# Performance work log

Measured on AMD Instinct MI355X. Metric: run time of the kernel, lower is better.

## Reference

```python
import jax, jax.numpy as jnp
import numpy as np
from jax import lax

DN = ('NCHW', 'OIHW', 'NCHW')


def setup_inputs() -> dict:
    key = jax.random.key(0)
    k1, k2, k3, k4, k5, k6 = jax.random.split(key, 6)
    B, Ch, H, W = 16, 256, 32, 32   # two feature maps of 256 ch -> c = 512
    C = 2 * Ch
    return {
        'x1': jax.random.normal(k1, (B, Ch, H, W), dtype=jnp.float32),
        'x2': jax.random.normal(k2, (B, Ch, H, W), dtype=jnp.float32),
        'g_w': jax.random.normal(k3, (C, C, 3, 3), dtype=jnp.float32) * 0.02,
        'w_w': jax.random.normal(k4, (256, C, 1, 1), dtype=jnp.float32) * 0.05,
        'weight1': jax.random.normal(k5, (C, 16), dtype=jnp.float32) * 0.1,
        'weight2': jax.random.normal(k6, (C, 16), dtype=jnp.float32) * 0.1,
    }


def reference(x1, x2, g_w, w_w, weight1, weight2):
    x = jnp.concatenate([x1, x2], axis=1)            # [b, c, h, w]
    b, c, h, w = x.shape
    g_x = lax.conv_general_dilated(x, g_w, (1, 1), 'SAME', dimension_numbers=DN)
    value = g_x.reshape(b, c, h * w)                 # [b, c, n]
    q = x.reshape(b, c, h * w)                       # query == key source
    sim = jnp.einsum('bcn,bdn->bcd', q, q) * (float(c) ** -0.5)  # [b, c, c]
    random_map = weight1 @ weight2.T                 # [c, c]
    attn = jax.nn.softmax(sim + random_map[None], axis=-1)
    ctx = jnp.einsum('bcd,bdn->bcn', attn, value).reshape(b, c, h, w)
    out = lax.conv_general_dilated(ctx, w_w, (1, 1), 'VALID', dimension_numbers=DN)
    return out
```

## Files before the change

### kernel.cpp

```cpp
#include <hip/hip_runtime.h>
#include <math.h>

typedef float f32x4 __attribute__((ext_vector_type(4)));
typedef short s16x8 __attribute__((ext_vector_type(8)));
typedef unsigned int u32;
typedef unsigned short u16;
typedef u16 u16x4 __attribute__((ext_vector_type(4)));

static constexpr size_t OFF_XT    = 0;
static constexpr size_t OFF_XQ    = 4734976;
static constexpr size_t OFF_ATTNT = 4734976;
static constexpr size_t OFF_WATTN = 6832128;
static constexpr size_t OFF_P0    = 8929280;
static constexpr size_t OFF_P1    = 11026432;
static constexpr size_t OFF_VT    = 8929280;
static constexpr size_t OFF_WA    = 13123584;
static constexpr size_t OFF_RM    = 14303232;
static constexpr size_t OFF_WWB   = 14565376;

__device__ __forceinline__ u16 f2bf(float f) {
    u32 u = __float_as_uint(f);
    u32 r = (u + 0x7FFFu + ((u >> 16) & 1u)) >> 16;
    return (u16)r;
}
__device__ __forceinline__ float bf2f(u16 v) {
    return __uint_as_float(((u32)v) << 16);
}

__device__ __forceinline__ void gload_lds16(const void* g, void* l) {
    __builtin_amdgcn_global_load_lds(
        (const u32 __attribute__((address_space(1)))*)(uintptr_t)g,
        (u32 __attribute__((address_space(3)))*)(uintptr_t)l, 16, 0, 0);
}

__global__ __launch_bounds__(256) void prep_kernel(const float* __restrict__ x1,
                                                   const float* __restrict__ x2,
                                                   const float* __restrict__ gw,
                                                   const float* __restrict__ ww,
                                                   const float* __restrict__ w1,
                                                   const float* __restrict__ w2,
                                                   float* __restrict__ rm,
                                                   u16* __restrict__ wA,
                                                   u16* __restrict__ wwb,
                                                   u16* __restrict__ xT,
                                                   u16* __restrict__ xq) {
    __shared__ __attribute__((aligned(16))) u32 shm[4608];
    const int t = threadIdx.x;
    const int bid = blockIdx.x;

    if (bid < 512) {
        const int co = bid;
        const float* g = gw + (size_t)co * 4608;
        float* lf = (float*)shm;
#pragma unroll
        for (int i = 0; i < 18; ++i) lf[t + i * 256] = g[t + i * 256];
        __syncthreads();
        u16* dst = wA + (size_t)co * 4608;
#pragma unroll
        for (int i = 0; i < 18; ++i) {
            int k = t + i * 256;
            int r = k >> 9, ci = k & 511;
            dst[k] = f2bf(lf[ci * 9 + r]);
        }
    } else if (bid < 2560) {
        int xid = bid - 512;
        int nt = xid & 15;
        int cit = (xid >> 4) & 7;
        int b = xid >> 7;
        int n0 = nt * 64, ci0 = cit * 64;
        const float* src = (ci0 < 256) ? (x1 + ((size_t)(b * 256 + ci0)) * 1024)
                                       : (x2 + ((size_t)(b * 256 + ci0 - 256)) * 1024);
        u16* xqb = xq + ((size_t)(b * 512 + ci0)) * 1024;
        u16* lt = (u16*)shm;
#pragma unroll
        for (int p4 = 0; p4 < 4; ++p4) {
            int ch = (t >> 4) + p4 * 16;
            int px = (t & 15) * 4;
            float4 v = *(const float4*)&src[(size_t)ch * 1024 + n0 + px];
            u16x4 pk = {f2bf(v.x), f2bf(v.y), f2bf(v.z), f2bf(v.w)};
            *(u16x4*)&xqb[(size_t)ch * 1024 + n0 + px] = pk;
            lt[(px + 0) * 65 + ch] = pk[0];
            lt[(px + 1) * 65 + ch] = pk[1];
            lt[(px + 2) * 65 + ch] = pk[2];
            lt[(px + 3) * 65 + ch] = pk[3];
        }
        __syncthreads();
        {
            int px_l = t >> 2, c16 = (t & 3) * 16;
            int n = n0 + px_l;
            int y = n >> 5, x = n & 31;
            int p = (y + 1) * 34 + (x + 1);
            u16* dst = xT + ((size_t)b * 1156 + p) * 512 + ci0 + c16;
            *(s16x8*)&dst[0] = *(const s16x8*)&lt[px_l * 65 + c16];
            *(s16x8*)&dst[8] = *(const s16x8*)&lt[px_l * 65 + c16 + 8];
        }
    } else if (bid < 2576) {
        int b = bid - 2560;
        u16* base = xT + (size_t)b * 1156 * 512;
        s16x8 z = {0, 0, 0, 0, 0, 0, 0, 0};
        for (int idx = t; idx < 132 * 64; idx += 256) {
            int row = idx >> 6, seg = idx & 63;
            int p;
            if (row < 34) p = row;
            else if (row < 68) p = 1122 + (row - 34);
            else if (row < 100) p = (row - 67) * 34;
            else p = (row - 99) * 34 + 33;
            *(s16x8*)&base[(size_t)p * 512 + seg * 8] = z;
        }
    } else if (bid < 3600) {
        int idx = (bid - 2576) * 256 + t;
        int c = idx >> 9, d = idx & 511;
        float s = 0.f;
#pragma unroll
        for (int k = 0; k < 16; ++k) s = fmaf(w1[c * 16 + k], w2[d * 16 + k], s);
        rm[idx] = s;
    } else {
        int idx = (bid - 3600) * 256 + t;
        float4 v = ((const float4*)ww)[idx];
        u16x4 pk = {f2bf(v.x), f2bf(v.y), f2bf(v.z), f2bf(v.w)};
        *(u16x4*)&wwb[(size_t)idx * 4] = pk;
    }
}

__global__ __launch_bounds__(256) void sim_part(const u16* __restrict__ xq,
                                                u16* __restrict__ simP) {
    __shared__ __attribute__((aligned(16))) u16 smem[128 * 128];
    u16* As = smem;
    u16* Bs = smem + 128 * 64;
    const int b = blockIdx.z, m0 = blockIdx.y * 128;
    const int n0 = (blockIdx.x & 3) * 128, khalf = blockIdx.x >> 2;
    const int t = threadIdx.x, w = t >> 6, l = t & 63;
    const u16* xb = xq + (size_t)b * 512 * 1024 + khalf * 512;

    const u16 *agp[4], *bgp[4];
    u16 *ald[4], *bld[4];
#pragma unroll
    for (int i = 0; i < 4; ++i) {
        int rr = w * 8 + i * 32 + (l >> 3);
        int gi = (l & 7) ^ (rr & 7);
        agp[i] = xb + (size_t)(m0 + rr) * 1024 + gi * 8;
        bgp[i] = xb + (size_t)(n0 + rr) * 1024 + gi * 8;
        ald[i] = &As[(w * 8 + i * 32) * 64];
        bld[i] = &Bs[(w * 8 + i * 32) * 64];
    }

    f32x4 acc[4][4] = {};
    const int wm = (w >> 1) * 64, wn = (w & 1) * 64;

    for (int kt = 0; kt < 8; ++kt) {
        int ko = kt << 6;
        if (kt) __syncthreads();
#pragma unroll
        for (int i = 0; i < 4; ++i) gload_lds16(agp[i] + ko, ald[i]);
#pragma unroll
        for (int i = 0; i < 4; ++i) gload_lds16(bgp[i] + ko, bld[i]);
        __syncthreads();
#pragma unroll
        for (int kk = 0; kk < 2; ++kk) {
            int gbase = kk * 4 + (l >> 4);
            s16x8 af[4], bf[4];
#pragma unroll
            for (int i = 0; i < 4; ++i) {
                int row = wm + i * 16 + (l & 15);
                af[i] = *(const s16x8*)&As[row * 64 + ((gbase ^ (row & 7)) << 3)];
            }
#pragma unroll
            for (int j = 0; j < 4; ++j) {
                int row = wn + j * 16 + (l & 15);
                bf[j] = *(const s16x8*)&Bs[row * 64 + ((gbase ^ (row & 7)) << 3)];
            }
#pragma unroll
            for (int i = 0; i < 4; ++i)
#pragma unroll
                for (int j = 0; j < 4; ++j)
                    acc[i][j] = __builtin_amdgcn_mfma_f32_16x16x32_bf16(af[i], bf[j], acc[i][j], 0, 0, 0);
        }
    }

    __syncthreads();
    const int col = l & 15, r4 = (l >> 4) * 4;
#pragma unroll
    for (int i = 0; i < 4; ++i)
#pragma unroll
        for (int j = 0; j < 4; ++j) {
            int n_l = wn + j * 16 + col;
            int m_b = wm + i * 16 + r4;
            u16x4 pk = {f2bf(acc[i][j][0]), f2bf(acc[i][j][1]),
                        f2bf(acc[i][j][2]), f2bf(acc[i][j][3])};
            *(u16x4*)&smem[n_l * 128 + (m_b ^ ((n_l & 15) << 3))] = pk;
        }
    __syncthreads();
    u16* sTb = simP + (size_t)khalf * 4194304 + (size_t)b * 512 * 512;
    {
        int n_l = t >> 1;
#pragma unroll
        for (int rep = 0; rep < 8; ++rep) {
            int c0 = (((t & 1) + rep * 2) << 3);
            s16x8 v = *(const s16x8*)&smem[n_l * 128 + (c0 ^ ((n_l & 15) << 3))];
            *(s16x8*)&sTb[(size_t)(n0 + n_l) * 512 + m0 + c0] = v;
        }
    }
}

__global__ __launch_bounds__(256) void finish_kernel(const u16* __restrict__ p0,
                                                     const u16* __restrict__ p1,
                                                     const float* __restrict__ rm,
                                                     u16* __restrict__ attnT) {
    __shared__ float rml[32 * 513];
    __shared__ float scr[256];
    const int t = threadIdx.x;
    const int b = blockIdx.x >> 4, c0 = (blockIdx.x & 15) * 32;
    const int cl = t & 31, g = t >> 5;
    const float scale = 0.04419417382415922f;

    for (int idx = t; idx < 32 * 512; idx += 256) {
        int c_l = idx >> 9, d = idx & 511;
        rml[c_l * 513 + d] = rm[(size_t)(c0 + c_l) * 512 + d];
    }
    __syncthreads();

    const u16* q0 = p0 + (size_t)b * 262144 + c0 + cl;
    const u16* q1 = p1 + (size_t)b * 262144 + c0 + cl;
    u16* ap = attnT + (size_t)b * 262144 + c0 + cl;
    const float* rp = &rml[cl * 513];

    float e[64];
    float s = 0.f;
#pragma unroll
    for (int dd = 0; dd < 64; ++dd) {
        int d = g * 64 + dd;
        float v = (bf2f(q0[(size_t)d * 512]) + bf2f(q1[(size_t)d * 512])) * scale + rp[d];
        e[dd] = __expf(v);
        s += e[dd];
    }
    scr[t] = s;
    __syncthreads();
    float tot = 0.f;
#pragma unroll
    for (int k = 0; k < 8; ++k) tot += scr[k * 32 + cl];
    float inv = 1.f / tot;
#pragma unroll
    for (int dd = 0; dd < 64; ++dd) {
        int d = g * 64 + dd;
        ap[(size_t)d * 512] = f2bf(e[dd] * inv);
    }
}

__global__ __launch_bounds__(256) void conv_gemm(const u16* __restrict__ wA,
                                                 const u16* __restrict__ xT,
                                                 u16* __restrict__ vT) {
    __shared__ __attribute__((aligned(16))) u16 smem[128 * 128];
    u16* As = smem;
    u16* Bs = smem + 128 * 64;
    const int b = blockIdx.z, m0 = blockIdx.y * 128, n0 = blockIdx.x * 128;
    const int t = threadIdx.x, w = t >> 6, l = t & 63;
    const u16* xTb = xT + (size_t)b * 1156 * 512;

    int gi[4], pb[4];
    const u16* agp[4];
    u16 *ald[4], *bld[4];
#pragma unroll
    for (int i = 0; i < 4; ++i) {
        int rr = w * 8 + i * 32 + (l >> 3);
        gi[i] = (l & 7) ^ (rr & 7);
        agp[i] = wA + (size_t)(m0 + rr) * 4608 + gi[i] * 8;
        int n = n0 + rr;
        pb[i] = (n >> 5) * 34 + (n & 31);
        ald[i] = &As[(w * 8 + i * 32) * 64];
        bld[i] = &Bs[(w * 8 + i * 32) * 64];
    }

    f32x4 acc[4][4] = {};
    const int wm = (w >> 1) * 64, wn = (w & 1) * 64;

    for (int kt = 0; kt < 72; ++kt) {
        int r = kt >> 3, ci0k = (kt & 7) << 6;
        int rdiv3 = (r * 11) >> 5;
        int poff = rdiv3 * 34 + (r - rdiv3 * 3);
        int aofs = r * 512 + ci0k;
        if (kt) __syncthreads();
#pragma unroll
        for (int i = 0; i < 4; ++i) gload_lds16(agp[i] + aofs, ald[i]);
#pragma unroll
        for (int i = 0; i < 4; ++i)
            gload_lds16(xTb + (size_t)(pb[i] + poff) * 512 + ci0k + gi[i] * 8, bld[i]);
        __syncthreads();

#pragma unroll
        for (int kk = 0; kk < 2; ++kk) {
            int gbase = kk * 4 + (l >> 4);
            s16x8 af[4], bf[4];
#pragma unroll
            for (int i = 0; i < 4; ++i) {
                int row = wm + i * 16 + (l & 15);
                af[i] = *(const s16x8*)&As[row * 64 + ((gbase ^ (row & 7)) << 3)];
            }
#pragma unroll
            for (int j = 0; j < 4; ++j) {
                int row = wn + j * 16 + (l & 15);
                bf[j] = *(const s16x8*)&Bs[row * 64 + ((gbase ^ (row & 7)) << 3)];
            }
#pragma unroll
            for (int i = 0; i < 4; ++i)
#pragma unroll
                for (int j = 0; j < 4; ++j)
                    acc[i][j] = __builtin_amdgcn_mfma_f32_16x16x32_bf16(af[i], bf[j], acc[i][j], 0, 0, 0);
        }
    }

    __syncthreads();
    const int col = l & 15, r4 = (l >> 4) * 4;
#pragma unroll
    for (int i = 0; i < 4; ++i)
#pragma unroll
        for (int j = 0; j < 4; ++j) {
            int n_l = wn + j * 16 + col;
            int co_b = wm + i * 16 + r4;
            u16x4 pk = {f2bf(acc[i][j][0]), f2bf(acc[i][j][1]),
                        f2bf(acc[i][j][2]), f2bf(acc[i][j][3])};
            *(u16x4*)&smem[n_l * 128 + (co_b ^ ((n_l & 15) << 3))] = pk;
        }
    __syncthreads();
    u16* vTb = vT + (size_t)b * 1024 * 512;
    {
        int n_l = t >> 1;
#pragma unroll
        for (int rep = 0; rep < 8; ++rep) {
            int c0 = (((t & 1) + rep * 2) << 3);
            s16x8 v = *(const s16x8*)&smem[n_l * 128 + (c0 ^ ((n_l & 15) << 3))];
            *(s16x8*)&vTb[(size_t)(n0 + n_l) * 512 + m0 + c0] = v;
        }
    }
}

template <int MODE>
__global__ __launch_bounds__(256) void gemm_nt(const u16* __restrict__ A, size_t sA,
                                               const u16* __restrict__ B, size_t sB,
                                               void* __restrict__ Cv, size_t sC,
                                               int K, int ldc) {
    __shared__ __attribute__((aligned(16))) u16 As[128 * 64];
    __shared__ __attribute__((aligned(16))) u16 Bs[128 * 64];
    const int b = blockIdx.z, m0 = blockIdx.y * 128, n0 = blockIdx.x * 128;
    const int t = threadIdx.x, w = t >> 6, l = t & 63;
    const u16* Ab = A + (size_t)b * sA;
    const u16* Bb = B + (size_t)b * sB;

    const u16 *agp[4], *bgp[4];
    u16 *ald[4], *bld[4];
#pragma unroll
    for (int i = 0; i < 4; ++i) {
        int rr = w * 8 + i * 32 + (l >> 3);
        int gi = (l & 7) ^ (rr & 7);
        agp[i] = Ab + (size_t)(m0 + rr) * K + gi * 8;
        bgp[i] = Bb + (size_t)(n0 + rr) * K + gi * 8;
        ald[i] = &As[(w * 8 + i * 32) * 64];
        bld[i] = &Bs[(w * 8 + i * 32) * 64];
    }

    f32x4 acc[4][4] = {};
    const int wm = (w >> 1) * 64, wn = (w & 1) * 64;
    const int nkt = K >> 6;
    for (int kt = 0; kt < nkt; ++kt) {
        int ko = kt << 6;
        if (kt) __syncthreads();
#pragma unroll
        for (int i = 0; i < 4; ++i) gload_lds16(agp[i] + ko, ald[i]);
#pragma unroll
        for (int i = 0; i < 4; ++i) gload_lds16(bgp[i] + ko, bld[i]);
        __syncthreads();
#pragma unroll
        for (int kk = 0; kk < 2; ++kk) {
            int gbase = kk * 4 + (l >> 4);
            s16x8 af[4], bf[4];
#pragma unroll
            for (int i = 0; i < 4; ++i) {
                int row = wm + i * 16 + (l & 15);
                af[i] = *(const s16x8*)&As[row * 64 + ((gbase ^ (row & 7)) << 3)];
            }
#pragma unroll
            for (int j = 0; j < 4; ++j) {
                int row = wn + j * 16 + (l & 15);
                bf[j] = *(const s16x8*)&Bs[row * 64 + ((gbase ^ (row & 7)) << 3)];
            }
#pragma unroll
            for (int i = 0; i < 4; ++i)
#pragma unroll
                for (int j = 0; j < 4; ++j)
                    acc[i][j] = __builtin_amdgcn_mfma_f32_16x16x32_bf16(af[i], bf[j], acc[i][j], 0, 0, 0);
        }
    }

    const int col = l & 15, r4 = (l >> 4) * 4;
#pragma unroll
    for (int i = 0; i < 4; ++i)
#pragma unroll
        for (int j = 0; j < 4; ++j)
#pragma unroll
            for (int reg = 0; reg < 4; ++reg) {
                int m = m0 + wm + i * 16 + r4 + reg;
                int n = n0 + wn + j * 16 + col;
                if (MODE == 1) {
                    u16* C = (u16*)Cv + (size_t)b * sC;
                    C[(size_t)m * ldc + n] = f2bf(acc[i][j][reg]);
                } else {
                    float* C = (float*)Cv + (size_t)b * sC;
                    C[(size_t)m * ldc + n] = acc[i][j][reg];
                }
            }
}

extern "C" void kernel_launch(void* const* d_in, const int* in_sizes, int n_in,
                              void* d_out, int out_size, void* d_ws, size_t ws_size,
                              hipStream_t stream) {
    (void)in_sizes; (void)n_in; (void)out_size; (void)ws_size;
    const float* x1 = (const float*)d_in[0];
    const float* x2 = (const float*)d_in[1];
    const float* gw = (const float*)d_in[2];
    const float* ww = (const float*)d_in[3];
    const float* w1 = (const float*)d_in[4];
    const float* w2 = (const float*)d_in[5];
    float* out = (float*)d_out;
    float* ws = (float*)d_ws;

    u16* xT    = (u16*)(ws + OFF_XT);
    u16* xq    = (u16*)(ws + OFF_XQ);
    u16* attnT = (u16*)(ws + OFF_ATTNT);
    u16* wattn = (u16*)(ws + OFF_WATTN);
    u16* simP  = (u16*)(ws + OFF_P0);
    u16* p0    = (u16*)(ws + OFF_P0);
    u16* p1    = (u16*)(ws + OFF_P1);
    u16* vT    = (u16*)(ws + OFF_VT);
    u16* wA    = (u16*)(ws + OFF_WA);
    float* rm  = ws + OFF_RM;
    u16* wwb   = (u16*)(ws + OFF_WWB);

    prep_kernel<<<3728, 256, 0, stream>>>(x1, x2, gw, ww, w1, w2, rm, wA, wwb, xT, xq);
    sim_part<<<dim3(8, 4, 16), 256, 0, stream>>>(xq, simP);
    finish_kernel<<<256, 256, 0, stream>>>(p0, p1, rm, attnT);
    gemm_nt<1><<<dim3(4, 2, 16), 256, 0, stream>>>(
        wwb, 0, attnT, (size_t)512 * 512, wattn, (size_t)256 * 512, 512, 512);
    conv_gemm<<<dim3(8, 4, 16), 256, 0, stream>>>(wA, xT, vT);
    gemm_nt<2><<<dim3(8, 2, 16), 256, 0, stream>>>(
        wattn, (size_t)256 * 512, vT, (size_t)1024 * 512, out, (size_t)256 * 1024, 512, 1024);
}
```

Before: 222.3 us.

## Replace split-K sim GEMM with full-K blocks and XCD-aware batch mapping

```diff
diff --git a/kernel.cpp b/kernel.cpp
--- a/kernel.cpp
+++ b/kernel.cpp
@@ -12,7 +12,6 @@
 static constexpr size_t OFF_ATTNT = 4734976;
 static constexpr size_t OFF_WATTN = 6832128;
 static constexpr size_t OFF_P0    = 8929280;
-static constexpr size_t OFF_P1    = 11026432;
 static constexpr size_t OFF_VT    = 8929280;
 static constexpr size_t OFF_WA    = 13123584;
 static constexpr size_t OFF_RM    = 14303232;
@@ -122,15 +121,18 @@
     }
 }
 
-__global__ __launch_bounds__(256) void sim_part(const u16* __restrict__ xq,
-                                                u16* __restrict__ simP) {
+__global__ __launch_bounds__(256) void sim_full(const u16* __restrict__ xq,
+                                                u16* __restrict__ sT) {
     __shared__ __attribute__((aligned(16))) u16 smem[128 * 128];
     u16* As = smem;
     u16* Bs = smem + 128 * 64;
-    const int b = blockIdx.z, m0 = blockIdx.y * 128;
-    const int n0 = (blockIdx.x & 3) * 128, khalf = blockIdx.x >> 2;
+    const int flat = blockIdx.x;
+    const int xcd = flat & 7, slot = flat >> 3;
+    const int b = 2 * xcd + (slot >> 4);
+    const int s = slot & 15;
+    const int m0 = (s >> 2) * 128, n0 = (s & 3) * 128;
     const int t = threadIdx.x, w = t >> 6, l = t & 63;
-    const u16* xb = xq + (size_t)b * 512 * 1024 + khalf * 512;
+    const u16* xb = xq + (size_t)b * 512 * 1024;
 
     const u16 *agp[4], *bgp[4];
     u16 *ald[4], *bld[4];
@@ -147,7 +149,7 @@
     f32x4 acc[4][4] = {};
     const int wm = (w >> 1) * 64, wn = (w & 1) * 64;
 
-    for (int kt = 0; kt < 8; ++kt) {
+    for (int kt = 0; kt < 16; ++kt) {
         int ko = kt << 6;
         if (kt) __syncthreads();
 #pragma unroll
@@ -190,7 +192,7 @@
             *(u16x4*)&smem[n_l * 128 + (m_b ^ ((n_l & 15) << 3))] = pk;
         }
     __syncthreads();
-    u16* sTb = simP + (size_t)khalf * 4194304 + (size_t)b * 512 * 512;
+    u16* sTb = sT + (size_t)b * 512 * 512;
     {
         int n_l = t >> 1;
 #pragma unroll
@@ -202,8 +204,7 @@
     }
 }
 
-__global__ __launch_bounds__(256) void finish_kernel(const u16* __restrict__ p0,
-                                                     const u16* __restrict__ p1,
+__global__ __launch_bounds__(256) void finish_kernel(const u16* __restrict__ sim,
                                                      const float* __restrict__ rm,
                                                      u16* __restrict__ attnT) {
     __shared__ float rml[32 * 513];
@@ -219,8 +220,7 @@
     }
     __syncthreads();
 
-    const u16* q0 = p0 + (size_t)b * 262144 + c0 + cl;
-    const u16* q1 = p1 + (size_t)b * 262144 + c0 + cl;
+    const u16* q0 = sim + (size_t)b * 262144 + c0 + cl;
     u16* ap = attnT + (size_t)b * 262144 + c0 + cl;
     const float* rp = &rml[cl * 513];
 
@@ -229,7 +229,7 @@
 #pragma unroll
     for (int dd = 0; dd < 64; ++dd) {
         int d = g * 64 + dd;
-        float v = (bf2f(q0[(size_t)d * 512]) + bf2f(q1[(size_t)d * 512])) * scale + rp[d];
+        float v = bf2f(q0[(size_t)d * 512]) * scale + rp[d];
         e[dd] = __expf(v);
         s += e[dd];
     }
@@ -427,16 +427,14 @@
     u16* attnT = (u16*)(ws + OFF_ATTNT);
     u16* wattn = (u16*)(ws + OFF_WATTN);
     u16* simP  = (u16*)(ws + OFF_P0);
-    u16* p0    = (u16*)(ws + OFF_P0);
-    u16* p1    = (u16*)(ws + OFF_P1);
     u16* vT    = (u16*)(ws + OFF_VT);
     u16* wA    = (u16*)(ws + OFF_WA);
     float* rm  = ws + OFF_RM;
     u16* wwb   = (u16*)(ws + OFF_WWB);
 
     prep_kernel<<<3728, 256, 0, stream>>>(x1, x2, gw, ww, w1, w2, rm, wA, wwb, xT, xq);
-    sim_part<<<dim3(8, 4, 16), 256, 0, stream>>>(xq, simP);
-    finish_kernel<<<256, 256, 0, stream>>>(p0, p1, rm, attnT);
+    sim_full<<<256, 256, 0, stream>>>(xq, simP);
+    finish_kernel<<<256, 256, 0, stream>>>(simP, rm, attnT);
     gemm_nt<1><<<dim3(4, 2, 16), 256, 0, stream>>>(
         wwb, 0, attnT, (size_t)512 * 512, wattn, (size_t)256 * 512, 512, 512);
     conv_gemm<<<dim3(8, 4, 16), 256, 0, stream>>>(wA, xT, vT);
```

After: 228.6 us. 2.8% more time.
